# Kernel tuning notes

Measured on AMD Instinct MI355X. Metric: run time of the kernel, lower is better.

Reference implementation:

```python
import jax, jax.numpy as jnp
import numpy as np

D_MODEL = 1024
N_HEADS = 16
THETA = 10000.0


def _rope(x, token_positions):
    # x: (b, h, s, d_k); token_positions: (b, s)
    d_k = x.shape[-1]
    powers = jnp.arange(0, d_k, 2, dtype=jnp.float32) / d_k        # (d_k/2,)
    freqs = 1.0 / (THETA ** powers)
    ang = token_positions.astype(jnp.float32)[..., None] * freqs   # (b, s, d_k/2)
    cos = jnp.cos(ang)[:, None, :, :].astype(x.dtype)              # (b, 1, s, d_k/2)
    sin = jnp.sin(ang)[:, None, :, :].astype(x.dtype)
    x_even = x[..., ::2]
    x_odd = x[..., 1::2]
    r1 = x_even * cos - x_odd * sin
    r2 = x_even * sin + x_odd * cos
    # interleave back to (..., d_k)
    return jnp.stack([r1, r2], axis=-1).reshape(x.shape)


def reference(x, token_positions, wq, wk, wv, wo):
    B, S, D = x.shape
    H = N_HEADS
    d_k = D // H

    def proj(w):
        y = jnp.einsum('bsi,oi->bso', x, w)
        return y.reshape(B, S, H, d_k).transpose(0, 2, 1, 3)  # (b, h, s, d_k)

    q = _rope(proj(wq), token_positions)
    k = _rope(proj(wk), token_positions)
    v = proj(wv)

    scale = 1.0 / jnp.sqrt(jnp.asarray(d_k, dtype=x.dtype))
    score = jnp.einsum('bhqd,bhkd->bhqk', q, k) * scale  # (b, h, s, s)
    causal = jnp.tril(jnp.ones((S, S), dtype=bool))
    score = jnp.where(causal, score, -jnp.inf)
    probs = jax.nn.softmax(score, axis=-1)
    attn = jnp.einsum('bhqk,bhkd->bhqd', probs, v)
    attn = attn.transpose(0, 2, 1, 3).reshape(B, S, D)
    return jnp.einsum('bsi,oi->bso', attn, wo)


def setup_inputs() -> dict:
    key = jax.random.key(0)
    ks = jax.random.split(key, 6)
    B, S, D = 2, 2048, D_MODEL
    std = (2.0 / (D + D)) ** 0.5
    x = jax.random.normal(ks[0], (B, S, D), dtype=jnp.float32)
    token_positions = jnp.broadcast_to(jnp.arange(S, dtype=jnp.int32), (B, S))
    wq = jax.random.normal(ks[1], (D, D), dtype=jnp.float32) * std
    wk = jax.random.normal(ks[2], (D, D), dtype=jnp.float32) * std
    wv = jax.random.normal(ks[3], (D, D), dtype=jnp.float32) * std
    wo = jax.random.normal(ks[4], (D, D), dtype=jnp.float32) * std
    return {"x": x, "token_positions": token_positions, "wq": wq, "wk": wk, "wv": wv, "wo": wo}
```

## Files before the change

kernel.cpp:

```cpp
#include <hip/hip_runtime.h>
#include <hip/hip_bf16.h>

typedef unsigned short u16;
typedef unsigned int u32;
typedef short short8 __attribute__((ext_vector_type(8)));
typedef u16 u16x8 __attribute__((ext_vector_type(8)));
typedef u16 u16x4 __attribute__((ext_vector_type(4)));
typedef float f32x4 __attribute__((ext_vector_type(4)));

#define MFMA(a, b, c) __builtin_amdgcn_mfma_f32_16x16x32_bf16((a), (b), (c), 0, 0, 0)

#define QSCALE 0.18033688011112042f

__device__ __forceinline__ u16 f2bf(float f) {
  unsigned u = __float_as_uint(f);
  unsigned r = (u + 0x7fffu + ((u >> 16) & 1u)) >> 16;
  return (u16)r;
}
__device__ __forceinline__ float bf2f(u16 h) {
  return __uint_as_float(((unsigned)h) << 16);
}
__device__ __forceinline__ float exp2hw(float x) {
  float r;
  asm("v_exp_f32 %0, %1" : "=v"(r) : "v"(x));
  return r;
}
__device__ __forceinline__ u32 cvtpk(float lo, float hi) {
  u32 d;
  asm("v_cvt_pk_bf16_f32 %0, %1, %2" : "=v"(d) : "v"(lo), "v"(hi));
  return d;
}
__device__ __forceinline__ void async16(const void* g, void* l) {
  __builtin_amdgcn_global_load_lds(
      (const __attribute__((address_space(1))) void*)g,
      (__attribute__((address_space(3))) void*)l, 16, 0, 0);
}
#define WAITV(N) asm volatile("s_waitcnt vmcnt(" #N ")" ::: "memory")
#define WAITL0() asm volatile("s_waitcnt lgkmcnt(0)" ::: "memory")
#define BAR() __builtin_amdgcn_s_barrier()
#define PRIO1 __builtin_amdgcn_s_setprio(1)
#define PRIO0 __builtin_amdgcn_s_setprio(0)

__global__ __launch_bounds__(256) void convert_kernel(
    const float* __restrict__ x, const float* __restrict__ wq,
    const float* __restrict__ wk, const float* __restrict__ wv,
    const float* __restrict__ wo, u16* __restrict__ ws) {
  int blk = blockIdx.x;
  const float* src; u16* dst;
  if (blk < 2048)      { src = x;  dst = ws; }
  else if (blk < 2560) { src = wq; dst = ws + 4194304;               blk -= 2048; }
  else if (blk < 3072) { src = wk; dst = ws + 4194304 + 1048576;     blk -= 2560; }
  else if (blk < 3584) { src = wv; dst = ws + 4194304 + 2 * 1048576; blk -= 3072; }
  else                 { src = wo; dst = ws + 4194304 + 3 * 1048576; blk -= 3584; }
  int idx = (blk * 256 + threadIdx.x) * 8;
  float4 v0 = *(const float4*)(src + idx);
  float4 v1 = *(const float4*)(src + idx + 4);
  u16x8 o;
  o[0] = f2bf(v0.x); o[1] = f2bf(v0.y); o[2] = f2bf(v0.z); o[3] = f2bf(v0.w);
  o[4] = f2bf(v1.x); o[5] = f2bf(v1.y); o[6] = f2bf(v1.z); o[7] = f2bf(v1.w);
  *(u16x8*)(dst + idx) = o;
}

__global__ __launch_bounds__(256) void rope_table(const int* __restrict__ tp,
                                                  float* __restrict__ tab) {
  int t = blockIdx.x * 256 + threadIdx.x;
  int bs = t >> 5, p = t & 31;
  float freq = exp2hw(-(float)p * 0.4152410118609203f);
  float ang = (float)tp[bs] * freq;
  float sn, cs;
  sincosf(ang, &sn, &cs);
  tab[bs * 64 + p * 2] = cs;
  tab[bs * 64 + p * 2 + 1] = sn;
}

__global__ __launch_bounds__(512, 2) void gemm_qkv256(
    const u16* __restrict__ xb, const u16* __restrict__ wqb,
    const u16* __restrict__ wkb, const u16* __restrict__ wvb,
    const float* __restrict__ tab, u16* __restrict__ qb, u16* __restrict__ kb,
    u16* __restrict__ vt) {
  __shared__ u16 As[2][2][8192];
  __shared__ u16 Bs[2][2][8192];
  const int tid = threadIdx.x, lane = tid & 63, wid = tid >> 6;
  const int wm = wid >> 2, wn = wid & 3;
  const int g = lane >> 4, r = lane & 15;
  const int z = blockIdx.z;
  const u16* Ag = xb;
  const u16* Bg = (z == 0) ? wqb : (z == 1) ? wkb : wvb;
  const int rowBase = blockIdx.y << 8, colBase = blockIdx.x << 8;

  const int c0 = tid, c1 = tid + 512;
  const int sr0 = c0 >> 3, sk0 = ((c0 & 7) ^ (sr0 & 7)) * 8;
  const int sr1 = c1 >> 3, sk1 = ((c1 & 7) ^ (sr1 & 7)) * 8;

#define STG_A(BUF, H, T)                                                      \
  do {                                                                        \
    async16(Ag + (size_t)(rowBase + (H)*128 + sr0) * 1024 + (T)*64 + sk0,     \
            (char*)As[BUF][H] + c0 * 16);                                     \
    async16(Ag + (size_t)(rowBase + (H)*128 + sr1) * 1024 + (T)*64 + sk1,     \
            (char*)As[BUF][H] + c1 * 16);                                     \
  } while (0)
#define STG_B(BUF, H, T)                                                      \
  do {                                                                        \
    async16(Bg + (size_t)(colBase + (H)*128 + sr0) * 1024 + (T)*64 + sk0,     \
            (char*)Bs[BUF][H] + c0 * 16);                                     \
    async16(Bg + (size_t)(colBase + (H)*128 + sr1) * 1024 + (T)*64 + sk1,     \
            (char*)Bs[BUF][H] + c1 * 16);                                     \
  } while (0)

  f32x4 acc[8][4];
#pragma unroll
  for (int m = 0; m < 8; m++)
#pragma unroll
    for (int n = 0; n < 4; n++) acc[m][n] = (f32x4){0.f, 0.f, 0.f, 0.f};
  short8 af[4][2], bfr[2][2];

#define RD_A(CUR, MH)                                                         \
  do {                                                                        \
    _Pragma("unroll") for (int mi = 0; mi < 4; mi++) {                        \
      int ra = (MH)*64 + mi * 16 + r;                                         \
      const u16* p = As[CUR][wm] + ra * 64;                                   \
      int sw = (ra & 7) << 3;                                                 \
      af[mi][0] = *(const short8*)(p + ((g << 3) ^ sw));                      \
      af[mi][1] = *(const short8*)(p + (((4 + g) << 3) ^ sw));                \
    }                                                                         \
  } while (0)
#define RD_B(CUR, NP)                                                         \
  do {                                                                        \
    _Pragma("unroll") for (int ni = 0; ni < 2; ni++) {                        \
      int cb = wn * 64 + ((NP)*2 + ni) * 16 + r;                              \
      const u16* p = Bs[CUR][cb >> 7] + (cb & 127) * 64;                      \
      int sw = (cb & 7) << 3;                                                 \
      bfr[ni][0] = *(const short8*)(p + ((g << 3) ^ sw));                     \
      bfr[ni][1] = *(const short8*)(p + (((4 + g) << 3) ^ sw));               \
    }                                                                         \
  } while (0)
#define MM16(MH, NP)                                                          \
  do {                                                                        \
    _Pragma("unroll") for (int mi = 0; mi < 4; mi++)                          \
        _Pragma("unroll") for (int ni = 0; ni < 2; ni++) {                    \
      acc[(MH)*4 + mi][(NP)*2 + ni] =                                         \
          MFMA(af[mi][0], bfr[ni][0], acc[(MH)*4 + mi][(NP)*2 + ni]);         \
      acc[(MH)*4 + mi][(NP)*2 + ni] =                                         \
          MFMA(af[mi][1], bfr[ni][1], acc[(MH)*4 + mi][(NP)*2 + ni]);         \
    }                                                                         \
  } while (0)

  STG_A(0, 0, 0); STG_A(0, 1, 0); STG_B(0, 0, 0); STG_B(0, 1, 0);
  STG_A(1, 0, 1); STG_A(1, 1, 1);
  WAITV(4);
  BAR();

  for (int t = 0; t < 16; ++t) {
    const int cur = t & 1, nxt = cur ^ 1;
    RD_A(cur, 0); RD_B(cur, 0);
    if (t < 15) { STG_B(nxt, 0, t + 1); STG_B(nxt, 1, t + 1); }
    BAR(); WAITL0();
    PRIO1; MM16(0, 0); PRIO0; BAR();
    RD_B(cur, 1);
    BAR(); WAITL0();
    PRIO1; MM16(0, 1); PRIO0; BAR();
    RD_A(cur, 1);
    BAR(); WAITL0();
    PRIO1; MM16(1, 1); PRIO0; BAR();
    RD_B(cur, 0);
    if (t < 14) {
      STG_A(cur, 0, t + 2); STG_A(cur, 1, t + 2);
      WAITV(4);
    } else {
      WAITV(0);
    }
    BAR(); WAITL0();
    PRIO1; MM16(1, 0); PRIO0; BAR();
  }
#undef STG_A
#undef STG_B
#undef RD_A
#undef RD_B
#undef MM16

  if (z < 2) {
    u16* dst = z ? kb : qb;
    const float qs = z ? 1.0f : QSCALE;
#pragma unroll
    for (int m = 0; m < 8; m++)
#pragma unroll
      for (int n = 0; n < 4; n++) {
        const int col = colBase + wn * 64 + n * 16 + r;
        const int p2 = (col >> 1) & 31;
        const bool odd = col & 1;
#pragma unroll
        for (int i = 0; i < 4; i++) {
          const int row = rowBase + wm * 128 + m * 16 + g * 4 + i;
          float2 cssn = *(const float2*)(tab + row * 64 + p2 * 2);
          float v = acc[m][n][i];
          float part = __shfl_xor(v, 1);
          float res = odd ? (part * cssn.y + v * cssn.x)
                          : (v * cssn.x - part * cssn.y);
          dst[(size_t)row * 1024 + col] = f2bf(res * qs);
        }
      }
  } else {
#pragma unroll
    for (int m = 0; m < 8; m++)
#pragma unroll
      for (int n = 0; n < 4; n++)
#pragma unroll
        for (int i = 0; i < 4; i++) {
          int row = rowBase + wm * 128 + m * 16 + g * 4 + i;
          int col = colBase + wn * 64 + n * 16 + r;
          int b = row >> 11, s = row & 2047;
          vt[(size_t)((b * 16 + (col >> 6)) * 64 + (col & 63)) * 2048 + s] =
              f2bf(acc[m][n][i]);
        }
  }
}

__device__ __forceinline__ void gemm_tile(const u16* __restrict__ A,
                                          const u16* __restrict__ Bm, int K,
                                          int rowBase, int colBase, u16* As,
                                          u16* Bs, f32x4 acc[4][4]) {
  const int tid = threadIdx.x;
  const int lane = tid & 63, wid = tid >> 6;
  const int wr = wid >> 1, wc = wid & 1;
  const int g = lane >> 4, r = lane & 15;

#pragma unroll
  for (int m = 0; m < 4; m++)
#pragma unroll
    for (int n = 0; n < 4; n++) acc[m][n] = (f32x4){0.f, 0.f, 0.f, 0.f};

#define GSTAGE(KT, BUF)                                                       \
  do {                                                                        \
    _Pragma("unroll") for (int i_ = 0; i_ < 4; ++i_) {                        \
      int c = i_ * 256 + tid;                                                 \
      int row = c >> 3, kc = (c & 7) ^ (row & 7);                             \
      async16(A + (size_t)(rowBase + row) * K + ((KT) << 6) + kc * 8,         \
              (char*)As + (BUF)*16384 + c * 16);                              \
    }                                                                         \
    _Pragma("unroll") for (int i_ = 0; i_ < 4; ++i_) {                        \
      int c = i_ * 256 + tid;                                                 \
      int row = c >> 3, kc = (c & 7) ^ (row & 7);                             \
      async16(Bm + (size_t)(colBase + row) * K + ((KT) << 6) + kc * 8,        \
              (char*)Bs + (BUF)*16384 + c * 16);                              \
    }                                                                         \
  } while (0)

  const int nkt = K >> 6;
  GSTAGE(0, 0);
  for (int kt = 0; kt < nkt; ++kt) {
    const int cur = kt & 1;
    if (kt + 1 < nkt) {
      GSTAGE(kt + 1, cur ^ 1);
      WAITV(8);
    } else {
      WAITV(0);
    }
    BAR();
    const u16* Ab = As + cur * 8192;
    const u16* Bb = Bs + cur * 8192;
#pragma unroll
    for (int ks = 0; ks < 2; ++ks) {
      short8 af[4], bfr[4];
#pragma unroll
      for (int m = 0; m < 4; m++) {
        int rr = wr * 64 + m * 16 + r;
        af[m] = *(const short8*)(Ab + rr * 64 + (((ks * 4 + g) ^ (rr & 7)) << 3));
      }
#pragma unroll
      for (int n = 0; n < 4; n++) {
        int rr = wc * 64 + n * 16 + r;
        bfr[n] = *(const short8*)(Bb + rr * 64 + (((ks * 4 + g) ^ (rr & 7)) << 3));
      }
#pragma unroll
      for (int m = 0; m < 4; m++)
#pragma unroll
        for (int n = 0; n < 4; n++)
          acc[m][n] = MFMA(af[m], bfr[n], acc[m][n]);
    }
    WAITL0();
    BAR();
  }
#undef GSTAGE
}

__global__ __launch_bounds__(256) void attn_kernel(const u16* __restrict__ qg,
                                                   const u16* __restrict__ kg,
                                                   const u16* __restrict__ vt,
                                                   u16* __restrict__ ab) {
  __shared__ u16 Ks[2][64 * 64];
  __shared__ u16 Vs[2][64 * 64];
  __shared__ u16 Ps[8][1024];
  const int tid = threadIdx.x, wid = tid >> 6, lane = tid & 63;
  const int g = lane >> 4, r = lane & 15;
  const int ak = blockIdx.x >> 5, bh = blockIdx.x & 31;
  const int a = ak >> 1, k = ak & 1;
  const int b = bh >> 4, h = bh & 15;
  const int rb[2] = {(a << 7) + (k << 6) + wid * 16,
                     ((15 - a) << 7) + (k << 6) + wid * 16};
  const int jend = 30 - 2 * a + k;

  short8 bq[2][2];
#pragma unroll
  for (int g2 = 0; g2 < 2; g2++) {
    const u16* qp =
        qg + (size_t)((b << 11) + rb[g2] + r) * 1024 + (h << 6) + g * 8;
    bq[g2][0] = *(const short8*)qp;
    bq[g2][1] = *(const short8*)(qp + 32);
  }

  f32x4 accO[2][4];
  float m_r[2] = {-1e30f, -1e30f}, l_r[2] = {0.f, 0.f};
#pragma unroll
  for (int g2 = 0; g2 < 2; g2++)
#pragma unroll
    for (int md = 0; md < 4; md++) accO[g2][md] = (f32x4){0.f, 0.f, 0.f, 0.f};

#define STAGE(JT, BUF)                                                        \
  do {                                                                        \
    _Pragma("unroll") for (int i_ = 0; i_ < 2; i_++) {                        \
      int c = i_ * 256 + tid;                                                 \
      int row = c >> 3, cc = (c & 7) ^ (row & 7);                             \
      async16(kg + (size_t)((b << 11) + ((JT) << 6) + row) * 1024 +           \
                  (h << 6) + cc * 8,                                          \
              (char*)Ks[BUF] + c * 16);                                       \
      async16(vt + (size_t)((bh << 6) + row) * 2048 + ((JT) << 6) + cc * 8,   \
              (char*)Vs[BUF] + c * 16);                                       \
    }                                                                         \
  } while (0)

  STAGE(0, 0);

  for (int j = 0; j <= jend; ++j) {
    const int cur = j & 1;
    if (j < jend) {
      STAGE(j + 1, cur ^ 1);
      WAITV(4);
    } else {
      WAITV(0);
    }
    BAR();
    const bool act0 = (j <= (rb[0] >> 6));
    const bool act1 = (j <= (rb[1] >> 6));
    if (act0 | act1) {
      const u16* Kb = Ks[cur];
      const u16* Vb = Vs[cur];
      short8 kf[4][2];
#pragma unroll
      for (int mk = 0; mk < 4; mk++) {
        kf[mk][0] = *(const short8*)(Kb + (mk * 16 + r) * 64 + ((g) ^ (r & 7)) * 8);
        kf[mk][1] = *(const short8*)(Kb + (mk * 16 + r) * 64 + ((4 + g) ^ (r & 7)) * 8);
      }
#pragma unroll
      for (int g2 = 0; g2 < 2; g2++) {
        if (!(g2 ? act1 : act0)) continue;
        f32x4 accS[4];
        PRIO1;
#pragma unroll
        for (int mk = 0; mk < 4; mk++) {
          f32x4 z = {0.f, 0.f, 0.f, 0.f};
          z = MFMA(kf[mk][0], bq[g2][0], z);
          z = MFMA(kf[mk][1], bq[g2][1], z);
          accS[mk] = z;
        }
        PRIO0;
        const int qrow = rb[g2] + r;
        if (j == (rb[g2] >> 6)) {
#pragma unroll
          for (int mk = 0; mk < 4; mk++)
#pragma unroll
            for (int i = 0; i < 4; i++)
              if ((j << 6) + mk * 16 + g * 4 + i > qrow) accS[mk][i] = -1e30f;
        }
        float pmax = accS[0][0];
#pragma unroll
        for (int mk = 0; mk < 4; mk++)
#pragma unroll
          for (int i = 0; i < 4; i++) pmax = fmaxf(pmax, accS[mk][i]);
        pmax = fmaxf(pmax, __shfl_xor(pmax, 16));
        pmax = fmaxf(pmax, __shfl_xor(pmax, 32));
        float mnew = m_r[g2];
        if (!__all(pmax <= mnew + 8.0f)) {
          mnew = fmaxf(mnew, pmax);
          float sc = exp2hw(m_r[g2] - mnew);
          l_r[g2] *= sc;
#pragma unroll
          for (int md = 0; md < 4; md++) accO[g2][md] *= sc;
          m_r[g2] = mnew;
        }
        float rs = 0.f;
        u16* pw = Ps[wid * 2 + g2];
#pragma unroll
        for (int mk = 0; mk < 4; mk++) {
          float p0 = exp2hw(accS[mk][0] - mnew);
          float p1 = exp2hw(accS[mk][1] - mnew);
          float p2 = exp2hw(accS[mk][2] - mnew);
          float p3 = exp2hw(accS[mk][3] - mnew);
          rs += (p0 + p1) + (p2 + p3);
          u32 d0 = cvtpk(p0, p1), d1 = cvtpk(p2, p3);
          uint2 dd = {d0, d1};
          *(uint2*)((char*)pw + r * 128 +
                    (((mk * 2 + (g >> 1)) ^ (r & 7)) << 4) + ((g & 1) << 3)) = dd;
        }
        rs += __shfl_xor(rs, 16);
        rs += __shfl_xor(rs, 32);
        l_r[g2] += rs;
      }
      WAITL0();
      short8 vf[4][2];
#pragma unroll
      for (int md = 0; md < 4; md++) {
        vf[md][0] = *(const short8*)(Vb + (md * 16 + r) * 64 + ((g) ^ (r & 7)) * 8);
        vf[md][1] = *(const short8*)(Vb + (md * 16 + r) * 64 + ((4 + g) ^ (r & 7)) * 8);
      }
      PRIO1;
#pragma unroll
      for (int g2 = 0; g2 < 2; g2++) {
        if (!(g2 ? act1 : act0)) continue;
        const u16* pw = Ps[wid * 2 + g2];
        short8 pb0 = *(const short8*)((const char*)pw + r * 128 + (((g) ^ (r & 7)) << 4));
        short8 pb1 = *(const short8*)((const char*)pw + r * 128 + (((4 + g) ^ (r & 7)) << 4));
#pragma unroll
        for (int md = 0; md < 4; md++) {
          accO[g2][md] = MFMA(vf[md][0], pb0, accO[g2][md]);
          accO[g2][md] = MFMA(vf[md][1], pb1, accO[g2][md]);
        }
      }
      PRIO0;
    }
    WAITL0();
    BAR();
  }
#undef STAGE

#pragma unroll
  for (int g2 = 0; g2 < 2; g2++) {
    float inv = 1.0f / l_r[g2];
#pragma unroll
    for (int md = 0; md < 4; md++) {
      u16x4 o;
#pragma unroll
      for (int i = 0; i < 4; i++) o[i] = f2bf(accO[g2][md][i] * inv);
      *(u16x4*)(ab + (size_t)((b << 11) + rb[g2] + r) * 1024 + (h << 6) +
                md * 16 + g * 4) = o;
    }
  }
}

__global__ __launch_bounds__(256) void gemm_ao(const u16* __restrict__ ab,
                                               const u16* __restrict__ wob,
                                               float* __restrict__ out) {
  __shared__ u16 As[2][128 * 64], Bs[2][128 * 64];
  f32x4 acc[4][4];
  gemm_tile(ab, wob, 1024, blockIdx.y * 128, blockIdx.x * 128, As[0], Bs[0], acc);
  const int lane = threadIdx.x & 63, wid = threadIdx.x >> 6;
  const int wr = wid >> 1, wc = wid & 1, g = lane >> 4, r = lane & 15;
  const int rowB = blockIdx.y * 128 + wr * 64;
  const int colB = blockIdx.x * 128 + wc * 64;
#pragma unroll
  for (int m = 0; m < 4; m++)
#pragma unroll
    for (int n = 0; n < 4; n++)
#pragma unroll
      for (int i = 0; i < 4; i++)
        out[(size_t)(rowB + m * 16 + g * 4 + i) * 1024 + colB + n * 16 + r] =
            acc[m][n][i];
}

extern "C" void kernel_launch(void* const* d_in, const int* in_sizes, int n_in,
                              void* d_out, int out_size, void* d_ws,
                              size_t ws_size, hipStream_t stream) {
  const float* x = (const float*)d_in[0];
  const int* tp = (const int*)d_in[1];
  const float* wq = (const float*)d_in[2];
  const float* wk = (const float*)d_in[3];
  const float* wv = (const float*)d_in[4];
  const float* wo = (const float*)d_in[5];
  float* out = (float*)d_out;

  u16* ws = (u16*)d_ws;
  u16* xb = ws;
  u16* wqb = xb + 4194304;
  u16* wkb = wqb + 1048576;
  u16* wvb = wkb + 1048576;
  u16* wob = wvb + 1048576;
  u16* qb = wob + 1048576;
  u16* kb = qb + 4194304;
  u16* vtb = kb + 4194304;
  u16* ab = vtb + 4194304;
  float* tab = (float*)ab;

  convert_kernel<<<4096, 256, 0, stream>>>(x, wq, wk, wv, wo, ws);
  rope_table<<<512, 256, 0, stream>>>(tp, tab);
  gemm_qkv256<<<dim3(4, 16, 3), 512, 0, stream>>>(xb, wqb, wkb, wvb, tab, qb,
                                                  kb, vtb);
  attn_kernel<<<512, 256, 0, stream>>>(qb, kb, vtb, ab);
  gemm_ao<<<dim3(8, 32), 256, 0, stream>>>(ab, wob, out);
}
```

Baseline: 124.8 us.

## Switch attention to 32x32 MFMA with register-resident P and merge GEMM phases

Rewrites the attention kernel so each wave handles 32 query rows with 32x32x16 bf16 MFMAs. The probability tile stays in registers, rearranged with v_permlane32_swap, which removes the LDS round-trip through the Ps buffer and cuts LDS usage. The kernel also declares two blocks per CU in its launch bounds. Separately, the QKV GEMM loop loads both B halves up front and fuses MFMA phases, leaving fewer barriers per k-step at the cost of more live registers. The causal masking and row-block work split are also reworked, which risks correctness bugs in the lane mapping.

```diff
diff --git a/kernel.cpp b/kernel.cpp
--- a/kernel.cpp
+++ b/kernel.cpp
@@ -6,9 +6,12 @@
 typedef short short8 __attribute__((ext_vector_type(8)));
 typedef u16 u16x8 __attribute__((ext_vector_type(8)));
 typedef u16 u16x4 __attribute__((ext_vector_type(4)));
+typedef u32 u32x4 __attribute__((ext_vector_type(4)));
 typedef float f32x4 __attribute__((ext_vector_type(4)));
+typedef float f32x16 __attribute__((ext_vector_type(16)));
 
 #define MFMA(a, b, c) __builtin_amdgcn_mfma_f32_16x16x32_bf16((a), (b), (c), 0, 0, 0)
+#define MFMA32(a, b, c) __builtin_amdgcn_mfma_f32_32x32x16_bf16((a), (b), (c), 0, 0, 0)
 
 #define QSCALE 0.18033688011112042f
 
@@ -30,10 +33,19 @@
   asm("v_cvt_pk_bf16_f32 %0, %1, %2" : "=v"(d) : "v"(lo), "v"(hi));
   return d;
 }
+__device__ __forceinline__ void plswap(u32& a, u32& b) {
+  asm volatile("v_permlane32_swap_b32 %0, %1" : "+v"(a), "+v"(b));
+}
 __device__ __forceinline__ void async16(const void* g, void* l) {
   __builtin_amdgcn_global_load_lds(
       (const __attribute__((address_space(1))) void*)g,
       (__attribute__((address_space(3))) void*)l, 16, 0, 0);
+}
+__device__ __forceinline__ f32x16 zero16() {
+  f32x16 z;
+#pragma unroll
+  for (int i = 0; i < 16; i++) z[i] = 0.f;
+  return z;
 }
 #define WAITV(N) asm volatile("s_waitcnt vmcnt(" #N ")" ::: "memory")
 #define WAITL0() asm volatile("s_waitcnt lgkmcnt(0)" ::: "memory")
@@ -112,7 +124,7 @@
   for (int m = 0; m < 8; m++)
 #pragma unroll
     for (int n = 0; n < 4; n++) acc[m][n] = (f32x4){0.f, 0.f, 0.f, 0.f};
-  short8 af[4][2], bfr[2][2];
+  short8 af[4][2], bfr[4][2];
 
 #define RD_A(CUR, MH)                                                         \
   do {                                                                        \
@@ -130,18 +142,18 @@
       int cb = wn * 64 + ((NP)*2 + ni) * 16 + r;                              \
       const u16* p = Bs[CUR][cb >> 7] + (cb & 127) * 64;                      \
       int sw = (cb & 7) << 3;                                                 \
-      bfr[ni][0] = *(const short8*)(p + ((g << 3) ^ sw));                     \
-      bfr[ni][1] = *(const short8*)(p + (((4 + g) << 3) ^ sw));               \
+      bfr[(NP)*2 + ni][0] = *(const short8*)(p + ((g << 3) ^ sw));            \
+      bfr[(NP)*2 + ni][1] = *(const short8*)(p + (((4 + g) << 3) ^ sw));      \
     }                                                                         \
   } while (0)
 #define MM16(MH, NP)                                                          \
   do {                                                                        \
     _Pragma("unroll") for (int mi = 0; mi < 4; mi++)                          \
         _Pragma("unroll") for (int ni = 0; ni < 2; ni++) {                    \
-      acc[(MH)*4 + mi][(NP)*2 + ni] =                                         \
-          MFMA(af[mi][0], bfr[ni][0], acc[(MH)*4 + mi][(NP)*2 + ni]);         \
-      acc[(MH)*4 + mi][(NP)*2 + ni] =                                         \
-          MFMA(af[mi][1], bfr[ni][1], acc[(MH)*4 + mi][(NP)*2 + ni]);         \
+      acc[(MH)*4 + mi][(NP)*2 + ni] = MFMA(af[mi][0], bfr[(NP)*2 + ni][0],    \
+                                           acc[(MH)*4 + mi][(NP)*2 + ni]);    \
+      acc[(MH)*4 + mi][(NP)*2 + ni] = MFMA(af[mi][1], bfr[(NP)*2 + ni][1],    \
+                                           acc[(MH)*4 + mi][(NP)*2 + ni]);    \
     }                                                                         \
   } while (0)
 
@@ -152,17 +164,12 @@
 
   for (int t = 0; t < 16; ++t) {
     const int cur = t & 1, nxt = cur ^ 1;
-    RD_A(cur, 0); RD_B(cur, 0);
+    RD_A(cur, 0);
+    RD_B(cur, 0); RD_B(cur, 1);
     if (t < 15) { STG_B(nxt, 0, t + 1); STG_B(nxt, 1, t + 1); }
     BAR(); WAITL0();
-    PRIO1; MM16(0, 0); PRIO0; BAR();
-    RD_B(cur, 1);
-    BAR(); WAITL0();
-    PRIO1; MM16(0, 1); PRIO0; BAR();
+    PRIO1; MM16(0, 0); MM16(0, 1); PRIO0; BAR();
     RD_A(cur, 1);
-    BAR(); WAITL0();
-    PRIO1; MM16(1, 1); PRIO0; BAR();
-    RD_B(cur, 0);
     if (t < 14) {
       STG_A(cur, 0, t + 2); STG_A(cur, 1, t + 2);
       WAITV(4);
@@ -170,7 +177,7 @@
       WAITV(0);
     }
     BAR(); WAITL0();
-    PRIO1; MM16(1, 0); PRIO0; BAR();
+    PRIO1; MM16(1, 0); MM16(1, 1); PRIO0; BAR();
   }
 #undef STG_A
 #undef STG_B
@@ -283,37 +290,32 @@
 #undef GSTAGE
 }
 
-__global__ __launch_bounds__(256) void attn_kernel(const u16* __restrict__ qg,
-                                                   const u16* __restrict__ kg,
-                                                   const u16* __restrict__ vt,
-                                                   u16* __restrict__ ab) {
+__global__ __launch_bounds__(256, 2) void attn_kernel(
+    const u16* __restrict__ qg, const u16* __restrict__ kg,
+    const u16* __restrict__ vt, u16* __restrict__ ab) {
   __shared__ u16 Ks[2][64 * 64];
   __shared__ u16 Vs[2][64 * 64];
-  __shared__ u16 Ps[8][1024];
   const int tid = threadIdx.x, wid = tid >> 6, lane = tid & 63;
-  const int g = lane >> 4, r = lane & 15;
+  const int q5 = lane & 31, hi = lane >> 5;
   const int ak = blockIdx.x >> 5, bh = blockIdx.x & 31;
   const int a = ak >> 1, k = ak & 1;
   const int b = bh >> 4, h = bh & 15;
-  const int rb[2] = {(a << 7) + (k << 6) + wid * 16,
-                     ((15 - a) << 7) + (k << 6) + wid * 16};
+  const int base = (wid < 2) ? a : (15 - a);
+  const int rb = base * 128 + k * 64 + (wid & 1) * 32;
+  const int cmax = rb >> 5;
   const int jend = 30 - 2 * a + k;
-
-  short8 bq[2][2];
-#pragma unroll
-  for (int g2 = 0; g2 < 2; g2++) {
-    const u16* qp =
-        qg + (size_t)((b << 11) + rb[g2] + r) * 1024 + (h << 6) + g * 8;
-    bq[g2][0] = *(const short8*)qp;
-    bq[g2][1] = *(const short8*)(qp + 32);
+  const int qrow = (b << 11) + rb + q5;
+
+  short8 bq[4];
+  {
+    const u16* qp = qg + (size_t)qrow * 1024 + (h << 6) + hi * 8;
+    bq[0] = *(const short8*)(qp);
+    bq[1] = *(const short8*)(qp + 16);
+    bq[2] = *(const short8*)(qp + 32);
+    bq[3] = *(const short8*)(qp + 48);
   }
-
-  f32x4 accO[2][4];
-  float m_r[2] = {-1e30f, -1e30f}, l_r[2] = {0.f, 0.f};
-#pragma unroll
-  for (int g2 = 0; g2 < 2; g2++)
-#pragma unroll
-    for (int md = 0; md < 4; md++) accO[g2][md] = (f32x4){0.f, 0.f, 0.f, 0.f};
+  f32x16 accO0 = zero16(), accO1 = zero16();
+  float m_r = -1e30f, l_r = 0.f;
 
 #define STAGE(JT, BUF)                                                        \
   do {                                                                        \
@@ -339,110 +341,128 @@
       WAITV(0);
     }
     BAR();
-    const bool act0 = (j <= (rb[0] >> 6));
-    const bool act1 = (j <= (rb[1] >> 6));
-    if (act0 | act1) {
+    if (2 * j <= cmax) {
       const u16* Kb = Ks[cur];
       const u16* Vb = Vs[cur];
-      short8 kf[4][2];
-#pragma unroll
-      for (int mk = 0; mk < 4; mk++) {
-        kf[mk][0] = *(const short8*)(Kb + (mk * 16 + r) * 64 + ((g) ^ (r & 7)) * 8);
-        kf[mk][1] = *(const short8*)(Kb + (mk * 16 + r) * 64 + ((4 + g) ^ (r & 7)) * 8);
-      }
-#pragma unroll
-      for (int g2 = 0; g2 < 2; g2++) {
-        if (!(g2 ? act1 : act0)) continue;
-        f32x4 accS[4];
+      const bool has1 = (2 * j + 1 <= cmax);
+      const int rsw = (q5 & 7) << 3;
+      f32x16 s0 = zero16(), s1 = zero16();
+      PRIO1;
+#pragma unroll
+      for (int kk = 0; kk < 4; kk++) {
+        short8 kf =
+            *(const short8*)(Kb + q5 * 64 + ((((kk << 1) + hi) << 3) ^ rsw));
+        s0 = MFMA32(kf, bq[kk], s0);
+      }
+      PRIO0;
+      if (has1) {
         PRIO1;
 #pragma unroll
-        for (int mk = 0; mk < 4; mk++) {
-          f32x4 z = {0.f, 0.f, 0.f, 0.f};
-          z = MFMA(kf[mk][0], bq[g2][0], z);
-          z = MFMA(kf[mk][1], bq[g2][1], z);
-          accS[mk] = z;
+        for (int kk = 0; kk < 4; kk++) {
+          short8 kf = *(const short8*)(Kb + (32 + q5) * 64 +
+                                       ((((kk << 1) + hi) << 3) ^ rsw));
+          s1 = MFMA32(kf, bq[kk], s1);
         }
         PRIO0;
-        const int qrow = rb[g2] + r;
-        if (j == (rb[g2] >> 6)) {
-#pragma unroll
-          for (int mk = 0; mk < 4; mk++)
-#pragma unroll
-            for (int i = 0; i < 4; i++)
-              if ((j << 6) + mk * 16 + g * 4 + i > qrow) accS[mk][i] = -1e30f;
+      }
+      if (2 * j == cmax) {
+#pragma unroll
+        for (int rg = 0; rg < 16; rg++) {
+          int rowk = (rg & 3) + 8 * (rg >> 2) + 4 * hi;
+          if (rowk > q5) s0[rg] = -1e30f;
         }
-        float pmax = accS[0][0];
-#pragma unroll
-        for (int mk = 0; mk < 4; mk++)
-#pragma unroll
-          for (int i = 0; i < 4; i++) pmax = fmaxf(pmax, accS[mk][i]);
-        pmax = fmaxf(pmax, __shfl_xor(pmax, 16));
-        pmax = fmaxf(pmax, __shfl_xor(pmax, 32));
-        float mnew = m_r[g2];
-        if (!__all(pmax <= mnew + 8.0f)) {
-          mnew = fmaxf(mnew, pmax);
-          float sc = exp2hw(m_r[g2] - mnew);
-          l_r[g2] *= sc;
-#pragma unroll
-          for (int md = 0; md < 4; md++) accO[g2][md] *= sc;
-          m_r[g2] = mnew;
+      } else if (2 * j + 1 == cmax) {
+#pragma unroll
+        for (int rg = 0; rg < 16; rg++) {
+          int rowk = (rg & 3) + 8 * (rg >> 2) + 4 * hi;
+          if (rowk > q5) s1[rg] = -1e30f;
         }
-        float rs = 0.f;
-        u16* pw = Ps[wid * 2 + g2];
-#pragma unroll
-        for (int mk = 0; mk < 4; mk++) {
-          float p0 = exp2hw(accS[mk][0] - mnew);
-          float p1 = exp2hw(accS[mk][1] - mnew);
-          float p2 = exp2hw(accS[mk][2] - mnew);
-          float p3 = exp2hw(accS[mk][3] - mnew);
-          rs += (p0 + p1) + (p2 + p3);
-          u32 d0 = cvtpk(p0, p1), d1 = cvtpk(p2, p3);
-          uint2 dd = {d0, d1};
-          *(uint2*)((char*)pw + r * 128 +
-                    (((mk * 2 + (g >> 1)) ^ (r & 7)) << 4) + ((g & 1) << 3)) = dd;
+      }
+      float pmax = s0[0];
+#pragma unroll
+      for (int rg = 1; rg < 16; rg++) pmax = fmaxf(pmax, s0[rg]);
+      if (has1) {
+#pragma unroll
+        for (int rg = 0; rg < 16; rg++) pmax = fmaxf(pmax, s1[rg]);
+      }
+      pmax = fmaxf(pmax, __shfl_xor(pmax, 32));
+      if (!__all(pmax <= m_r + 8.0f)) {
+        float mn = fmaxf(m_r, pmax);
+        float sc = exp2hw(m_r - mn);
+        l_r *= sc;
+#pragma unroll
+        for (int rg = 0; rg < 16; rg++) {
+          accO0[rg] *= sc;
+          accO1[rg] *= sc;
         }
-        rs += __shfl_xor(rs, 16);
-        rs += __shfl_xor(rs, 32);
-        l_r[g2] += rs;
-      }
-      WAITL0();
-      short8 vf[4][2];
-#pragma unroll
-      for (int md = 0; md < 4; md++) {
-        vf[md][0] = *(const short8*)(Vb + (md * 16 + r) * 64 + ((g) ^ (r & 7)) * 8);
-        vf[md][1] = *(const short8*)(Vb + (md * 16 + r) * 64 + ((4 + g) ^ (r & 7)) * 8);
-      }
+        m_r = mn;
+      }
+      float rs = 0.f;
+      u32 pw00[4], pw01[4], pw10[4], pw11[4];
+#define PACK(SREG, OUT, S16)                                                  \
+  do {                                                                        \
+    float p0 = exp2hw(SREG[(S16)*8 + 0] - m_r);                               \
+    float p1 = exp2hw(SREG[(S16)*8 + 1] - m_r);                               \
+    float p2 = exp2hw(SREG[(S16)*8 + 2] - m_r);                               \
+    float p3 = exp2hw(SREG[(S16)*8 + 3] - m_r);                               \
+    float p4 = exp2hw(SREG[(S16)*8 + 4] - m_r);                               \
+    float p5 = exp2hw(SREG[(S16)*8 + 5] - m_r);                               \
+    float p6 = exp2hw(SREG[(S16)*8 + 6] - m_r);                               \
+    float p7 = exp2hw(SREG[(S16)*8 + 7] - m_r);                               \
+    rs += ((p0 + p1) + (p2 + p3)) + ((p4 + p5) + (p6 + p7));                  \
+    u32 X = cvtpk(p0, p1), Y = cvtpk(p2, p3);                                 \
+    u32 U = cvtpk(p4, p5), W = cvtpk(p6, p7);                                 \
+    plswap(X, U);                                                             \
+    plswap(Y, W);                                                             \
+    OUT[0] = X; OUT[1] = Y; OUT[2] = U; OUT[3] = W;                           \
+  } while (0)
+      PACK(s0, pw00, 0);
+      PACK(s0, pw01, 1);
+      if (has1) {
+        PACK(s1, pw10, 0);
+        PACK(s1, pw11, 1);
+      }
+#undef PACK
+      rs += __shfl_xor(rs, 32);
+      l_r += rs;
+#define PVSTEP(PW, CH)                                                        \
+  do {                                                                        \
+    u32x4 pv_ = {PW[0], PW[1], PW[2], PW[3]};                                 \
+    short8 pb_ = __builtin_bit_cast(short8, pv_);                             \
+    short8 v0_ =                                                              \
+        *(const short8*)(Vb + q5 * 64 + ((((CH) + hi) << 3) ^ rsw));          \
+    short8 v1_ = *(const short8*)(Vb + (32 + q5) * 64 +                       \
+                                  ((((CH) + hi) << 3) ^ rsw));                \
+    accO0 = MFMA32(v0_, pb_, accO0);                                          \
+    accO1 = MFMA32(v1_, pb_, accO1);                                          \
+  } while (0)
       PRIO1;
-#pragma unroll
-      for (int g2 = 0; g2 < 2; g2++) {
-        if (!(g2 ? act1 : act0)) continue;
-        const u16* pw = Ps[wid * 2 + g2];
-        short8 pb0 = *(const short8*)((const char*)pw + r * 128 + (((g) ^ (r & 7)) << 4));
-        short8 pb1 = *(const short8*)((const char*)pw + r * 128 + (((4 + g) ^ (r & 7)) << 4));
-#pragma unroll
-        for (int md = 0; md < 4; md++) {
-          accO[g2][md] = MFMA(vf[md][0], pb0, accO[g2][md]);
-          accO[g2][md] = MFMA(vf[md][1], pb1, accO[g2][md]);
-        }
+      PVSTEP(pw00, 0);
+      PVSTEP(pw01, 2);
+      if (has1) {
+        PVSTEP(pw10, 4);
+        PVSTEP(pw11, 6);
       }
       PRIO0;
+#undef PVSTEP
     }
     WAITL0();
     BAR();
   }
 #undef STAGE
 
-#pragma unroll
-  for (int g2 = 0; g2 < 2; g2++) {
-    float inv = 1.0f / l_r[g2];
-#pragma unroll
-    for (int md = 0; md < 4; md++) {
-      u16x4 o;
-#pragma unroll
-      for (int i = 0; i < 4; i++) o[i] = f2bf(accO[g2][md][i] * inv);
-      *(u16x4*)(ab + (size_t)((b << 11) + rb[g2] + r) * 1024 + (h << 6) +
-                md * 16 + g * 4) = o;
+  float inv = 1.0f / l_r;
+#pragma unroll
+  for (int qd = 0; qd < 4; qd++) {
+    u16x4 o0, o1;
+#pragma unroll
+    for (int e = 0; e < 4; e++) {
+      o0[e] = f2bf(accO0[qd * 4 + e] * inv);
+      o1[e] = f2bf(accO1[qd * 4 + e] * inv);
     }
+    u16* op = ab + (size_t)qrow * 1024 + (h << 6) + qd * 8 + hi * 4;
+    *(u16x4*)(op) = o0;
+    *(u16x4*)(op + 32) = o1;
   }
 }
 
```

Result: no change. 124.1 us (-0.6%).
